# Kernel tuning notes

Measured on AMD Instinct MI355X. Metric: run time of the kernel, lower is better.

The kernel has to match this reference:

```python
import jax, jax.numpy as jnp
import numpy as np

N_NODES = 50000
N_EDGES = 400000
F_IN = 128
HID = 64
HEADS = 8
N_CLASSES = 16
NEG_SLOPE = 0.2  # PyG GATConv default negative_slope


def _glorot(key, shape):
    fan_in, fan_out = shape[0], shape[-1]
    lim = jnp.sqrt(6.0 / (fan_in + fan_out))
    return jax.random.uniform(key, shape, jnp.float32, -lim, lim)


def setup_inputs() -> dict:
    key = jax.random.key(0)
    ks = jax.random.split(key, 16)
    x = jax.random.normal(ks[0], (N_NODES, F_IN), jnp.float32)
    edge_index = jax.random.randint(ks[1], (2, N_EDGES), 0, N_NODES, jnp.int64)
    # layer 0: F_IN -> HEADS*HID (concat)
    W0 = _glorot(ks[2], (F_IN, HEADS * HID))
    a_s0 = _glorot(ks[3], (HEADS, HID))
    a_d0 = _glorot(ks[4], (HEADS, HID))
    b0 = jnp.zeros((HEADS * HID,), jnp.float32)
    # layer 1: HEADS*HID -> HEADS*HID (concat)
    W1 = _glorot(ks[5], (HEADS * HID, HEADS * HID))
    a_s1 = _glorot(ks[6], (HEADS, HID))
    a_d1 = _glorot(ks[7], (HEADS, HID))
    b1 = jnp.zeros((HEADS * HID,), jnp.float32)
    # final layer: HEADS*HID -> N_CLASSES, heads=1, concat=False (mean over heads)
    W2 = _glorot(ks[8], (HEADS * HID, 1 * N_CLASSES))
    a_s2 = _glorot(ks[9], (1, N_CLASSES))
    a_d2 = _glorot(ks[10], (1, N_CLASSES))
    b2 = jnp.zeros((N_CLASSES,), jnp.float32)
    return {"x": x, "edge_index": edge_index,
            "W0": W0, "a_s0": a_s0, "a_d0": a_d0, "b0": b0,
            "W1": W1, "a_s1": a_s1, "a_d1": a_d1, "b1": b1,
            "W2": W2, "a_s2": a_s2, "a_d2": a_d2, "b2": b2}


def gat_conv(x, src, dst, W, a_src, a_dst, b, num_nodes, concat):
    """One PyG-style GATConv (self-loops already in src/dst).
    x: [N, F_in]; W: [F_in, H*C]; a_src/a_dst: [H, C]; b: [H*C] or [C]."""
    H, C = a_src.shape
    h = (x @ W).reshape(num_nodes, H, C)                    # [N,H,C]
    al_s = jnp.einsum('nhc,hc->nh', h, a_src)               # [N,H]
    al_d = jnp.einsum('nhc,hc->nh', h, a_dst)               # [N,H]
    e = jax.nn.leaky_relu(al_s[src] + al_d[dst], NEG_SLOPE) # [E,H]
    # scatter-softmax over incoming edges of each destination node
    m = jax.ops.segment_max(e, dst, num_segments=num_nodes)  # [N,H]
    ex = jnp.exp(e - m[dst])
    denom = jax.ops.segment_sum(ex, dst, num_segments=num_nodes)
    alpha = ex / denom[dst]                                  # [E,H]
    out = jax.ops.segment_sum(alpha[:, :, None] * h[src], dst,
                              num_segments=num_nodes)        # [N,H,C]
    if concat:
        return out.reshape(num_nodes, H * C) + b
    return out.mean(axis=1) + b


def reference(x, edge_index, W0, a_s0, a_d0, b0, W1, a_s1, a_d1, b1,
              W2, a_s2, a_d2, b2):
    N = x.shape[0]
    # PyG GATConv adds self-loops by default
    loops = jnp.arange(N, dtype=edge_index.dtype)
    src = jnp.concatenate([edge_index[0], loops])
    dst = jnp.concatenate([edge_index[1], loops])
    h = gat_conv(x, src, dst, W0, a_s0, a_d0, b0, N, concat=True)
    h = jax.nn.elu(h)  # dropout is identity in eval mode
    h = gat_conv(h, src, dst, W1, a_s1, a_d1, b1, N, concat=True)
    h = jax.nn.elu(h)
    return gat_conv(h, src, dst, W2, a_s2, a_d2, b2, N, concat=False)
```

## Files before the change

kernel.cpp:

```cpp
#include <hip/hip_runtime.h>

#define N_NODES 50000
#define N_EDGES 400000
#define E_TOT   450000
#define NEG 0.2f
#define NB_SCAN ((N_NODES + 255) / 256)
#define MAXD 64

typedef unsigned short ushort_t;
typedef __attribute__((ext_vector_type(8))) _Float16 half8;
typedef __attribute__((ext_vector_type(4))) float  f32x4;
typedef __attribute__((ext_vector_type(8))) unsigned short ushort8;

__device__ __forceinline__ ushort_t f2h(float f){
    _Float16 h = (_Float16)f;
    union { _Float16 h; ushort_t u; } v; v.h = h; return v.u;
}
__device__ __forceinline__ float h_lo(unsigned u){
    union { unsigned u; _Float16 h[2]; } v; v.u = u; return (float)v.h[0];
}
__device__ __forceinline__ float h_hi(unsigned u){
    union { unsigned u; _Float16 h[2]; } v; v.u = u; return (float)v.h[1];
}
__device__ __forceinline__ void gload_lds16(const void* g, void* l){
    __builtin_amdgcn_global_load_lds((const __attribute__((address_space(1))) void*)g,
                                     (__attribute__((address_space(3))) void*)l, 16, 0, 0);
}
__device__ __forceinline__ int wave_incl_scan(int v, int lane){
    #pragma unroll
    for(int off = 1; off < 64; off <<= 1){
        int t = __shfl_up(v, off, 64);
        if(lane >= off) v += t;
    }
    return v;
}


__global__ void cvt_all(const float* __restrict__ W0,
                        const float* __restrict__ W1, const float* __restrict__ W2,
                        const int* __restrict__ ei,
                        ushort_t* __restrict__ W0t,
                        ushort_t* __restrict__ W1t, ushort_t* __restrict__ W2t,
                        int* __restrict__ deg){
    int i = blockIdx.x*256 + threadIdx.x;
    if(i < 512*128){ int n = i >> 7, k = i & 127; W0t[i] = f2h(W0[(size_t)k*512 + n]); }
    if(i < 512*512){ int n = i >> 9, k = i & 511; W1t[i] = f2h(W1[(size_t)k*512 + n]); }
    if(i < 16*512){ int n = i >> 9, k = i & 511; W2t[i] = f2h(W2[(size_t)k*16 + n]); }
    if(i < E_TOT){
        int dst = (i < N_EDGES) ? ei[N_EDGES + i] : (i - N_EDGES);
        atomicAdd(&deg[dst], 1);
    }
}


__global__ void deg_block_sum(const int* __restrict__ deg, int* __restrict__ bsum){
    int i = blockIdx.x*256 + threadIdx.x;
    int lane = threadIdx.x & 63, wave = threadIdx.x >> 6;
    int v = (i < N_NODES) ? deg[i] : 0;
    #pragma unroll
    for(int off = 1; off < 64; off <<= 1) v += __shfl_xor(v, off, 64);
    __shared__ int sw[4];
    if(lane == 0) sw[wave] = v;
    __syncthreads();
    if(threadIdx.x == 0) bsum[blockIdx.x] = sw[0] + sw[1] + sw[2] + sw[3];
}

__global__ void scan_apply(const int* __restrict__ bsum,
                           int* __restrict__ dw, int* __restrict__ rowptr){
    __shared__ int soff;
    __shared__ int sw[4];
    int i = blockIdx.x*256 + threadIdx.x;
    int lane = threadIdx.x & 63, wave = threadIdx.x >> 6;
    if(wave == 0){
        int s = 0;
        for(int j = lane; j < (int)blockIdx.x; j += 64) s += bsum[j];
        #pragma unroll
        for(int off = 1; off < 64; off <<= 1) s += __shfl_xor(s, off, 64);
        if(lane == 0) soff = s;
    }
    int v = (i < N_NODES) ? dw[i] : 0;
    int incl = wave_incl_scan(v, lane);
    if(lane == 63) sw[wave] = incl;
    __syncthreads();
    int add = soff;
    for(int w = 0; w < wave; w++) add += sw[w];
    int excl = incl - v + add;
    if(i < N_NODES){ rowptr[i] = excl; dw[i] = excl; }
    if(i == N_NODES-1) rowptr[N_NODES] = excl + v;
}

__global__ void scatter_edges(const int* __restrict__ ei, int* __restrict__ wofs,
                              int* __restrict__ csr){
    int e = blockIdx.x*256 + threadIdx.x;
    if(e >= E_TOT) return;
    int src, dst;
    if(e < N_EDGES){ src = ei[e]; dst = ei[N_EDGES + e]; }
    else { src = dst = e - N_EDGES; }
    int pos = atomicAdd(&wofs[dst], 1);
    csr[pos] = src;
}


__global__ __launch_bounds__(512, 2) void gemm0f(const float* __restrict__ x,
                                                 const ushort_t* __restrict__ W0t,
                                                 ushort_t* __restrict__ Cb,
                                                 const float* __restrict__ a_s,
                                                 const float* __restrict__ a_d,
                                                 float* __restrict__ als,
                                                 float* __restrict__ ald, int M){
    extern __shared__ ushort_t lds[];
    ushort_t* As = lds;
    ushort_t* Bs = lds + 128*128;
    int tid = threadIdx.x, wave = tid >> 6, lane = tid & 63;
    int row0 = blockIdx.x * 128;

    {
        int rsub = lane >> 4, c16 = lane & 15;
        #pragma unroll
        for(int s = 0; s < 16; s++){
            int rowq = wave*64 + s*4;
            int r = rowq + rsub;
            int sc = c16 ^ (r & 7);
            gload_lds16(W0t + (size_t)r*128 + sc*8, Bs + rowq*128);
        }
    }
    {
        int rsub = lane >> 4, c16 = lane & 15;
        #pragma unroll
        for(int t = 0; t < 4; t++){
            int rl = wave*16 + t*4 + rsub;
            int gr = row0 + rl; gr = gr < M ? gr : M-1;
            const float* ap = x + (size_t)gr*128 + c16*8;
            f32x4 lo = *(const f32x4*)ap;
            f32x4 hi = *(const f32x4*)(ap + 4);
            union { _Float16 h[8]; half8 v; } u;
            u.h[0] = (_Float16)lo[0]; u.h[1] = (_Float16)lo[1];
            u.h[2] = (_Float16)lo[2]; u.h[3] = (_Float16)lo[3];
            u.h[4] = (_Float16)hi[0]; u.h[5] = (_Float16)hi[1];
            u.h[6] = (_Float16)hi[2]; u.h[7] = (_Float16)hi[3];
            *(half8*)&As[(size_t)rl*128 + (c16 ^ (rl & 7))*8] = u.v;
        }
    }

    __syncthreads();

    f32x4 acc[8][4] = {};
    int fm = lane & 15, fq = lane >> 4;
    #pragma unroll
    for(int kt = 0; kt < 4; kt++){
        half8 a[8], b[4];
        #pragma unroll
        for(int mi = 0; mi < 8; mi++){
            int r = mi*16 + fm;
            a[mi] = *(const half8*)&As[(size_t)r*128 + ((kt*4 + fq) ^ (r & 7))*8];
        }
        #pragma unroll
        for(int nj = 0; nj < 4; nj++){
            int r = wave*64 + nj*16 + fm;
            b[nj] = *(const half8*)&Bs[(size_t)r*128 + ((kt*4 + fq) ^ (r & 7))*8];
        }
        #pragma unroll
        for(int mi = 0; mi < 8; mi++)
            #pragma unroll
            for(int nj = 0; nj < 4; nj++)
                acc[mi][nj] = __builtin_amdgcn_mfma_f32_16x16x32_f16(a[mi], b[nj], acc[mi][nj], 0, 0, 0);
    }

    int head = wave;
    float asv[4], adv[4];
    #pragma unroll
    for(int nj = 0; nj < 4; nj++){
        int c = head*64 + nj*16 + fm;
        asv[nj] = a_s[c]; adv[nj] = a_d[c];
    }
    #pragma unroll
    for(int mi = 0; mi < 8; mi++){
        #pragma unroll
        for(int p2 = 0; p2 < 4; p2++){
            int r = row0 + mi*16 + fq*4 + p2;
            float ps = 0.f, pd = 0.f;
            if(r < M){
                ushort_t* cp = &Cb[(size_t)r*512 + head*64 + fm];
                #pragma unroll
                for(int nj = 0; nj < 4; nj++){
                    float v = acc[mi][nj][p2];
                    cp[nj*16] = f2h(v);
                    ps += v*asv[nj]; pd += v*adv[nj];
                }
            }
            #pragma unroll
            for(int off = 1; off < 16; off <<= 1){
                ps += __shfl_xor(ps, off);
                pd += __shfl_xor(pd, off);
            }
            if(fm == 0 && r < M){ als[r*8 + head] = ps; ald[r*8 + head] = pd; }
        }
    }
}


template<int K>
__global__ __launch_bounds__(512, 2) void gemm_bt8(const ushort_t* __restrict__ A,
                                                   const ushort_t* __restrict__ Bt,
                                                   ushort_t* __restrict__ Cb,
                                                   const float* __restrict__ a_s,
                                                   const float* __restrict__ a_d,
                                                   float* __restrict__ als,
                                                   float* __restrict__ ald, int M){
    extern __shared__ ushort_t lds[];
    constexpr int NT = K / 64;
    int tid = threadIdx.x, wave = tid >> 6, lane = tid & 63;
    int wm = wave >> 2, wn = wave & 3;

    int s = blockIdx.x, nb = gridDim.x;
    int cc = s & 7, kk = s >> 3;
    int q = nb >> 3, rr = nb & 7;
    int t = (cc < rr ? cc*(q+1) : rr*(q+1) + (cc-rr)*q) + kk;
    int row0 = (t >> 1) * 256;
    int col0 = (t & 1) * 256;

    int lr = lane >> 3;
    int cs8 = ((lane & 7) ^ lr) << 3;
    int arows[4], brows[4];
    #pragma unroll
    for(int i = 0; i < 4; i++){
        int r = row0 + (wave << 5) + (i << 3) + lr;
        arows[i] = r < M ? r : M-1;
        brows[i] = col0 + (wave << 5) + (i << 3) + lr;
    }

    int l15 = lane & 15, fq = lane >> 4;
    int xr = (lane & 7) << 4;
    int xco0 = ((fq << 4)      ) ^ xr;
    int xco1 = (64 | (fq << 4)) ^ xr;

    f32x4 acc[8][4] = {};

    auto stage = [&](int nbuf, int kt, int i){
        ushort_t* la = lds + nbuf*16384 + (wave << 11) + (i << 9);
        ushort_t* lb = lds + 32768 + nbuf*16384 + (wave << 11) + (i << 9);
        gload_lds16(A  + (size_t)arows[i]*K + kt + cs8, la);
        gload_lds16(Bt + (size_t)brows[i]*K + kt + cs8, lb);
    };

    #pragma unroll
    for(int i = 0; i < 4; i++) stage(0, 0, i);
    #pragma unroll
    for(int i = 0; i < 4; i++) stage(1, 64, i);

    for(int it = 0; it < NT; ++it){
        int b = it & 1;
        if(it < NT-1) asm volatile("s_waitcnt vmcnt(8)" ::: "memory");
        else         asm volatile("s_waitcnt vmcnt(0)" ::: "memory");
        __builtin_amdgcn_s_barrier();
        const char* Ac = (const char*)(lds + b*16384);
        const char* Bc = (const char*)(lds + 32768 + b*16384);
        #pragma unroll
        for(int p = 0; p < 4; ++p){
            half8 aF[2][2], bF[4][2];
            #pragma unroll
            for(int m2 = 0; m2 < 2; m2++){
                int ro = (((wm << 7) + (((p << 1) | m2) << 4) + l15)) << 7;
                aF[m2][0] = *(const half8*)(Ac + ro + xco0);
                aF[m2][1] = *(const half8*)(Ac + ro + xco1);
            }
            #pragma unroll
            for(int nj = 0; nj < 4; nj++){
                int ro = (((wn << 6) + (nj << 4) + l15)) << 7;
                bF[nj][0] = *(const half8*)(Bc + ro + xco0);
                bF[nj][1] = *(const half8*)(Bc + ro + xco1);
            }
            if(p == 3) asm volatile("s_waitcnt lgkmcnt(0)" ::: "memory");
            __builtin_amdgcn_s_barrier();
            if(p == 3 && it < NT-2){
                #pragma unroll
                for(int i = 0; i < 4; i++) stage(b, (it + 2) << 6, i);
            }
            __builtin_amdgcn_s_setprio(1);
            #pragma unroll
            for(int m2 = 0; m2 < 2; m2++)
                #pragma unroll
                for(int nj = 0; nj < 4; nj++){
                    acc[(p<<1)|m2][nj] = __builtin_amdgcn_mfma_f32_16x16x32_f16(aF[m2][0], bF[nj][0], acc[(p<<1)|m2][nj], 0, 0, 0);
                    acc[(p<<1)|m2][nj] = __builtin_amdgcn_mfma_f32_16x16x32_f16(aF[m2][1], bF[nj][1], acc[(p<<1)|m2][nj], 0, 0, 0);
                }
            __builtin_amdgcn_s_setprio(0);
            __builtin_amdgcn_s_barrier();
        }
    }

    int head = (col0 >> 6) + wn;
    float asv[4], adv[4];
    #pragma unroll
    for(int nj = 0; nj < 4; nj++){
        int c = (head << 6) + (nj << 4) + l15;
        asv[nj] = a_s[c]; adv[nj] = a_d[c];
    }
    #pragma unroll
    for(int mi = 0; mi < 8; mi++){
        #pragma unroll
        for(int p2 = 0; p2 < 4; p2++){
            int r = row0 + (wm << 7) + (mi << 4) + (fq << 2) + p2;
            float ps = 0.f, pd = 0.f;
            if(r < M){
                ushort_t* cp = &Cb[(size_t)r*512 + (head << 6) + l15];
                #pragma unroll
                for(int nj = 0; nj < 4; nj++){
                    float v = acc[mi][nj][p2];
                    cp[nj << 4] = f2h(v);
                    ps += v*asv[nj]; pd += v*adv[nj];
                }
            }
            #pragma unroll
            for(int off = 1; off < 16; off <<= 1){
                ps += __shfl_xor(ps, off);
                pd += __shfl_xor(pd, off);
            }
            if(l15 == 0 && r < M){ als[r*8 + head] = ps; ald[r*8 + head] = pd; }
        }
    }
}


__global__ __launch_bounds__(256) void attn_agg(const ushort_t* __restrict__ h,
        const float* __restrict__ als, const float* __restrict__ ald,
        const int* __restrict__ rowptr, const int* __restrict__ csr,
        const float* __restrict__ bias, ushort_t* __restrict__ out){
    __shared__ float sex[4][MAXD][8];
    int wv = threadIdx.x >> 6, lane = threadIdx.x & 63;
    int n = blockIdx.x*4 + wv;
    int start = rowptr[n], end = rowptr[n+1];

    int hd = lane & 7, e8 = lane >> 3;
    float aldv = ald[n*8 + hd];
    float lmax = -1e30f;
    for(int idx = start + e8; idx < end; idx += 8){
        int e = idx - start;
        int src = csr[idx];
        float v = als[src*8 + hd] + aldv;
        v = v > 0.f ? v : NEG*v;
        if(e < MAXD) sex[wv][e][hd] = v;
        lmax = fmaxf(lmax, v);
    }
    for(int off = 8; off < 64; off <<= 1) lmax = fmaxf(lmax, __shfl_xor(lmax, off));
    float lsum = 0.f;
    for(int idx = start + e8; idx < end; idx += 8){
        int e = idx - start;
        float v;
        if(e < MAXD) v = sex[wv][e][hd];
        else { int src = csr[idx]; v = als[src*8 + hd] + aldv; v = v > 0.f ? v : NEG*v; }
        float ex = __expf(v - lmax);
        if(e < MAXD) sex[wv][e][hd] = ex;
        lsum += ex;
    }
    for(int off = 8; off < 64; off <<= 1) lsum += __shfl_xor(lsum, off);

    int head = e8;
    float m_all = __shfl(lmax, head);
    float inv   = 1.f / __shfl(lsum, head);
    float aldn  = __shfl(aldv, head);

    float acc[8] = {};

    int cnt = end - start;
    int nmain = cnt < MAXD ? cnt : MAXD;
    int mend = start + nmain;
    int last = mend - 1;
    for(int idx = start; idx < mend; idx += 8){
        int ss[8]; uint4 pp[8]; float ee[8];
        #pragma unroll
        for(int k = 0; k < 8; k++){
            int j = idx + k;
            ss[k] = csr[j <= last ? j : last];
        }
        #pragma unroll
        for(int k = 0; k < 8; k++)
            pp[k] = *(const uint4*)&h[(size_t)ss[k]*512 + lane*8];
        #pragma unroll
        for(int k = 0; k < 8; k++){
            int j = idx + k;
            ee[k] = (j < mend) ? sex[wv][j-start][head] : 0.f;
        }
        #pragma unroll
        for(int k = 0; k < 8; k++){
            acc[0] += ee[k]*h_lo(pp[k].x); acc[1] += ee[k]*h_hi(pp[k].x);
            acc[2] += ee[k]*h_lo(pp[k].y); acc[3] += ee[k]*h_hi(pp[k].y);
            acc[4] += ee[k]*h_lo(pp[k].z); acc[5] += ee[k]*h_hi(pp[k].z);
            acc[6] += ee[k]*h_lo(pp[k].w); acc[7] += ee[k]*h_hi(pp[k].w);
        }
    }
    if(mend < end){
        for(int idx = mend; idx < end; idx++){
            int src = csr[idx];
            float v = als[src*8 + head] + aldn;
            v = v > 0.f ? v : NEG*v;
            float e0 = __expf(v - m_all);
            uint4 p = *(const uint4*)&h[(size_t)src*512 + lane*8];
            acc[0] += e0*h_lo(p.x); acc[1] += e0*h_hi(p.x);
            acc[2] += e0*h_lo(p.y); acc[3] += e0*h_hi(p.y);
            acc[4] += e0*h_lo(p.z); acc[5] += e0*h_hi(p.z);
            acc[6] += e0*h_lo(p.w); acc[7] += e0*h_hi(p.w);
        }
    }

    ushort8 o;
    #pragma unroll
    for(int j = 0; j < 8; j++){
        float v = acc[j]*inv + bias[lane*8 + j];
        v = v > 0.f ? v : (__expf(v) - 1.f);
        o[j] = f2h(v);
    }
    *(ushort8*)&out[(size_t)n*512 + lane*8] = o;
}


__global__ __launch_bounds__(256) void gemm2_mfma(const ushort_t* __restrict__ A,
                                                  const ushort_t* __restrict__ W2t,
                                                  const float* __restrict__ a_s2,
                                                  const float* __restrict__ a_d2,
                                                  float* __restrict__ C,
                                                  float* __restrict__ als,
                                                  float* __restrict__ ald){
    int wave = threadIdx.x >> 6, lane = threadIdx.x & 63;
    long row0 = (long)(blockIdx.x*4 + wave)*16;
    int fr = lane & 15, fq = lane >> 4;
    long ar = row0 + fr;
    if(ar > N_NODES-1) ar = N_NODES-1;
    const ushort_t* ap = A + ar*512 + fq*8;
    const ushort_t* bp = W2t + (size_t)fr*512 + fq*8;
    f32x4 acc = {};
    #pragma unroll
    for(int kt = 0; kt < 512; kt += 32){
        half8 a = *(const half8*)(ap + kt);
        half8 b = *(const half8*)(bp + kt);
        acc = __builtin_amdgcn_mfma_f32_16x16x32_f16(a, b, acc, 0, 0, 0);
    }
    float as_ = a_s2[fr], ad_ = a_d2[fr];
    #pragma unroll
    for(int p = 0; p < 4; p++){
        long r = row0 + fq*4 + p;
        float v = acc[p];
        float ps = v*as_, pd = v*ad_;
        #pragma unroll
        for(int off = 1; off < 16; off <<= 1){
            ps += __shfl_xor(ps, off);
            pd += __shfl_xor(pd, off);
        }
        if(r < N_NODES){
            C[r*16 + fr] = v;
            if(fr == 0){ als[r] = ps; ald[r] = pd; }
        }
    }
}

__global__ __launch_bounds__(256) void attn_agg2(const float* __restrict__ h2,
        const float* __restrict__ als, const float* __restrict__ ald,
        const int* __restrict__ rowptr, const int* __restrict__ csr,
        const float* __restrict__ b2, float* __restrict__ out){
    __shared__ float sex2[16][MAXD+1];
    int wv = threadIdx.x >> 6, lane = threadIdx.x & 63;
    int q = lane >> 4, c = lane & 15;
    int slot = wv*4 + q;
    int n = blockIdx.x*16 + slot;
    int start = rowptr[n], end = rowptr[n+1];
    float aldv = ald[n];
    int cnt = end - start;
    int nmain = cnt < MAXD ? cnt : MAXD;
    int mend = start + nmain;

    float lmax = -1e30f;
    for(int idx = start + c; idx < end; idx += 16){
        int e = idx - start;
        float v = als[csr[idx]] + aldv; v = v > 0.f ? v : NEG*v;
        if(e < MAXD) sex2[slot][e] = v;
        lmax = fmaxf(lmax, v);
    }
    #pragma unroll
    for(int off = 1; off < 16; off <<= 1) lmax = fmaxf(lmax, __shfl_xor(lmax, off));
    float lsum = 0.f;
    for(int idx = start + c; idx < end; idx += 16){
        int e = idx - start;
        float v;
        if(e < MAXD) v = sex2[slot][e];
        else { v = als[csr[idx]] + aldv; v = v > 0.f ? v : NEG*v; }
        float ex = __expf(v - lmax);
        if(e < MAXD) sex2[slot][e] = ex;
        lsum += ex;
    }
    #pragma unroll
    for(int off = 1; off < 16; off <<= 1) lsum += __shfl_xor(lsum, off);
    float inv = 1.f / lsum;

    float acc = 0.f;
    for(int idx = start; idx < mend; idx++){
        int src = csr[idx];
        float ex = sex2[slot][idx - start];
        acc += ex * h2[(size_t)src*16 + c];
    }
    for(int idx = mend; idx < end; idx++){
        int src = csr[idx];
        float v = als[src] + aldv; v = v > 0.f ? v : NEG*v;
        acc += __expf(v - lmax) * h2[(size_t)src*16 + c];
    }
    out[(size_t)n*16 + c] = acc*inv + b2[c];
}


extern "C" void kernel_launch(void* const* d_in, const int* in_sizes, int n_in,
                              void* d_out, int out_size, void* d_ws, size_t ws_size,
                              hipStream_t stream) {
    const float* x    = (const float*)d_in[0];
    const int*   ei   = (const int*)  d_in[1];
    const float* W0   = (const float*)d_in[2];
    const float* a_s0 = (const float*)d_in[3];
    const float* a_d0 = (const float*)d_in[4];
    const float* b0   = (const float*)d_in[5];
    const float* W1   = (const float*)d_in[6];
    const float* a_s1 = (const float*)d_in[7];
    const float* a_d1 = (const float*)d_in[8];
    const float* b1   = (const float*)d_in[9];
    const float* W2   = (const float*)d_in[10];
    const float* a_s2 = (const float*)d_in[11];
    const float* a_d2 = (const float*)d_in[12];
    const float* b2   = (const float*)d_in[13];
    float* out = (float*)d_out;

    char* w = (char*)d_ws;
    auto alloc = [&](size_t bytes){ void* p = (void*)w; w += (bytes + 255) & ~(size_t)255; return p; };
    int*      rowptr = (int*)     alloc((N_NODES+1)*sizeof(int));
    int*      wofs   = (int*)     alloc((N_NODES+1)*sizeof(int));
    int*      bsum   = (int*)     alloc(NB_SCAN*sizeof(int));
    int*      csr    = (int*)     alloc(E_TOT*sizeof(int));
    float*    als    = (float*)   alloc((size_t)N_NODES*8*sizeof(float));
    float*    ald    = (float*)   alloc((size_t)N_NODES*8*sizeof(float));
    float*    als2   = (float*)   alloc((size_t)N_NODES*sizeof(float));
    float*    ald2   = (float*)   alloc((size_t)N_NODES*sizeof(float));
    ushort_t* hb     = (ushort_t*)alloc((size_t)N_NODES*512*sizeof(ushort_t));
    ushort_t* hbf    = (ushort_t*)alloc((size_t)N_NODES*512*sizeof(ushort_t));
    ushort_t* W0t    = (ushort_t*)alloc((size_t)512*128*sizeof(ushort_t));
    ushort_t* W1t    = (ushort_t*)alloc((size_t)512*512*sizeof(ushort_t));
    ushort_t* W2t    = (ushort_t*)alloc((size_t)16*512*sizeof(ushort_t));
    float*    h2     = (float*)   alloc((size_t)N_NODES*16*sizeof(float));

    const int NBLK = 2 * ((N_NODES + 255) / 256);
    const int NG0  = (N_NODES + 127) / 128;

    (void)hipFuncSetAttribute((const void*)gemm_bt8<512>,
                              hipFuncAttributeMaxDynamicSharedMemorySize, 131072);
    (void)hipFuncSetAttribute((const void*)gemm0f,
                              hipFuncAttributeMaxDynamicSharedMemorySize, 163840);

    hipMemsetAsync(wofs, 0, (N_NODES+1)*sizeof(int), stream);
    cvt_all<<<(E_TOT+255)/256, 256, 0, stream>>>(W0, W1, W2, ei, W0t, W1t, W2t, wofs);

    deg_block_sum<<<NB_SCAN, 256, 0, stream>>>(wofs, bsum);
    scan_apply<<<NB_SCAN, 256, 0, stream>>>(bsum, wofs, rowptr);
    scatter_edges<<<(E_TOT+255)/256, 256, 0, stream>>>(ei, wofs, csr);

    gemm0f<<<NG0, 512, 163840, stream>>>(x, W0t, hb, a_s0, a_d0, als, ald, N_NODES);
    attn_agg<<<N_NODES/4, 256, 0, stream>>>(hb, als, ald, rowptr, csr, b0, hbf);

    gemm_bt8<512><<<NBLK, 512, 131072, stream>>>(hbf, W1t, hb, a_s1, a_d1, als, ald, N_NODES);
    attn_agg<<<N_NODES/4, 256, 0, stream>>>(hb, als, ald, rowptr, csr, b1, hbf);

    gemm2_mfma<<<(N_NODES+63)/64, 256, 0, stream>>>(hbf, W2t, a_s2, a_d2, h2, als2, ald2);
    attn_agg2<<<N_NODES/16, 256, 0, stream>>>(h2, als2, ald2, rowptr, csr, b2, out);
}
```

Before: 419.5 us.

## Fuse CSR edge scatter into layer-0 GEMM and process two row tiles per block

Removes the separate scatter_edges launch and folds the edge-to-CSR atomic scatter into the first GEMM kernel, with each block handling a slice of edges while its W0/x tiles load. Each GEMM block now covers 256 rows in two 128-row passes, so W0 is staged into LDS once per block and the next A tile is staged while the previous epilogue runs. The grid drops to 196 blocks at one block per CU. That cuts parallelism and latency hiding and serialises the two tiles inside each block, in exchange for one fewer launch and less W0 reloading.

```diff
diff --git a/kernel.cpp b/kernel.cpp
--- a/kernel.cpp
+++ b/kernel.cpp
@@ -6,6 +6,8 @@
 #define NEG 0.2f
 #define NB_SCAN ((N_NODES + 255) / 256)
 #define MAXD 64
+#define NG0 196
+#define EPB ((E_TOT + NG0 - 1) / NG0)
 
 typedef unsigned short ushort_t;
 typedef __attribute__((ext_vector_type(8))) _Float16 half8;
@@ -89,48 +91,31 @@
     if(i == N_NODES-1) rowptr[N_NODES] = excl + v;
 }
 
-__global__ void scatter_edges(const int* __restrict__ ei, int* __restrict__ wofs,
-                              int* __restrict__ csr){
-    int e = blockIdx.x*256 + threadIdx.x;
-    if(e >= E_TOT) return;
-    int src, dst;
-    if(e < N_EDGES){ src = ei[e]; dst = ei[N_EDGES + e]; }
-    else { src = dst = e - N_EDGES; }
-    int pos = atomicAdd(&wofs[dst], 1);
-    csr[pos] = src;
-}
-
-
-__global__ __launch_bounds__(512, 2) void gemm0f(const float* __restrict__ x,
-                                                 const ushort_t* __restrict__ W0t,
-                                                 ushort_t* __restrict__ Cb,
-                                                 const float* __restrict__ a_s,
-                                                 const float* __restrict__ a_d,
-                                                 float* __restrict__ als,
-                                                 float* __restrict__ ald, int M){
+
+__global__ __launch_bounds__(512, 1) void gemm0fs(const int* __restrict__ ei,
+                                                  int* __restrict__ wofs,
+                                                  int* __restrict__ csr,
+                                                  const float* __restrict__ x,
+                                                  const ushort_t* __restrict__ W0t,
+                                                  ushort_t* __restrict__ Cb,
+                                                  const float* __restrict__ a_s,
+                                                  const float* __restrict__ a_d,
+                                                  float* __restrict__ als,
+                                                  float* __restrict__ ald, int M){
     extern __shared__ ushort_t lds[];
-    ushort_t* As = lds;
-    ushort_t* Bs = lds + 128*128;
+    ushort_t* Bs = lds;
+    ushort_t* As = lds + 512*128;
     int tid = threadIdx.x, wave = tid >> 6, lane = tid & 63;
-    int row0 = blockIdx.x * 128;
-
-    {
-        int rsub = lane >> 4, c16 = lane & 15;
-        #pragma unroll
-        for(int s = 0; s < 16; s++){
-            int rowq = wave*64 + s*4;
-            int r = rowq + rsub;
-            int sc = c16 ^ (r & 7);
-            gload_lds16(W0t + (size_t)r*128 + sc*8, Bs + rowq*128);
-        }
-    }
-    {
-        int rsub = lane >> 4, c16 = lane & 15;
+    int rsub = lane >> 4, c16 = lane & 15;
+    int fm = lane & 15, fq = lane >> 4;
+    long row0 = (long)blockIdx.x * 256;
+
+    auto stageA = [&](long base){
         #pragma unroll
         for(int t = 0; t < 4; t++){
             int rl = wave*16 + t*4 + rsub;
-            int gr = row0 + rl; gr = gr < M ? gr : M-1;
-            const float* ap = x + (size_t)gr*128 + c16*8;
+            long gr = base + rl; gr = gr < M ? gr : M-1;
+            const float* ap = x + gr*128 + c16*8;
             f32x4 lo = *(const f32x4*)ap;
             f32x4 hi = *(const f32x4*)(ap + 4);
             union { _Float16 h[8]; half8 v; } u;
@@ -140,62 +125,93 @@
             u.h[6] = (_Float16)hi[2]; u.h[7] = (_Float16)hi[3];
             *(half8*)&As[(size_t)rl*128 + (c16 ^ (rl & 7))*8] = u.v;
         }
+    };
+    auto compute = [&](f32x4 (&acc)[8][4]){
+        #pragma unroll
+        for(int kt = 0; kt < 4; kt++){
+            half8 a[8], b[4];
+            #pragma unroll
+            for(int mi = 0; mi < 8; mi++){
+                int r = mi*16 + fm;
+                a[mi] = *(const half8*)&As[(size_t)r*128 + ((kt*4 + fq) ^ (r & 7))*8];
+            }
+            #pragma unroll
+            for(int nj = 0; nj < 4; nj++){
+                int r = wave*64 + nj*16 + fm;
+                b[nj] = *(const half8*)&Bs[(size_t)r*128 + ((kt*4 + fq) ^ (r & 7))*8];
+            }
+            #pragma unroll
+            for(int mi = 0; mi < 8; mi++)
+                #pragma unroll
+                for(int nj = 0; nj < 4; nj++)
+                    acc[mi][nj] = __builtin_amdgcn_mfma_f32_16x16x32_f16(a[mi], b[nj], acc[mi][nj], 0, 0, 0);
+        }
+    };
+    auto epilogue = [&](f32x4 (&acc)[8][4], long base){
+        int head = wave;
+        float asv[4], adv[4];
+        #pragma unroll
+        for(int nj = 0; nj < 4; nj++){
+            int c = head*64 + nj*16 + fm;
+            asv[nj] = a_s[c]; adv[nj] = a_d[c];
+        }
+        #pragma unroll
+        for(int mi = 0; mi < 8; mi++){
+            #pragma unroll
+            for(int p2 = 0; p2 < 4; p2++){
+                long r = base + mi*16 + fq*4 + p2;
+                float ps = 0.f, pd = 0.f;
+                if(r < M){
+                    ushort_t* cp = &Cb[(size_t)r*512 + head*64 + fm];
+                    #pragma unroll
+                    for(int nj = 0; nj < 4; nj++){
+                        float v = acc[mi][nj][p2];
+                        cp[nj*16] = f2h(v);
+                        ps += v*asv[nj]; pd += v*adv[nj];
+                    }
+                }
+                #pragma unroll
+                for(int off = 1; off < 16; off <<= 1){
+                    ps += __shfl_xor(ps, off);
+                    pd += __shfl_xor(pd, off);
+                }
+                if(fm == 0 && r < M){ als[r*8 + head] = ps; ald[r*8 + head] = pd; }
+            }
+        }
+    };
+
+    #pragma unroll
+    for(int s = 0; s < 16; s++){
+        int rowq = wave*64 + s*4;
+        int r = rowq + rsub;
+        int sc = c16 ^ (r & 7);
+        gload_lds16(W0t + (size_t)r*128 + sc*8, Bs + rowq*128);
+    }
+    stageA(row0);
+
+    {
+        int e1 = blockIdx.x*EPB + EPB; if(e1 > E_TOT) e1 = E_TOT;
+        for(int e = blockIdx.x*EPB + tid; e < e1; e += 512){
+            int src, dst;
+            if(e < N_EDGES){ src = ei[e]; dst = ei[N_EDGES + e]; }
+            else { src = dst = e - N_EDGES; }
+            int pos = atomicAdd(&wofs[dst], 1);
+            csr[pos] = src;
+        }
     }
 
     __syncthreads();
 
     f32x4 acc[8][4] = {};
-    int fm = lane & 15, fq = lane >> 4;
-    #pragma unroll
-    for(int kt = 0; kt < 4; kt++){
-        half8 a[8], b[4];
-        #pragma unroll
-        for(int mi = 0; mi < 8; mi++){
-            int r = mi*16 + fm;
-            a[mi] = *(const half8*)&As[(size_t)r*128 + ((kt*4 + fq) ^ (r & 7))*8];
-        }
-        #pragma unroll
-        for(int nj = 0; nj < 4; nj++){
-            int r = wave*64 + nj*16 + fm;
-            b[nj] = *(const half8*)&Bs[(size_t)r*128 + ((kt*4 + fq) ^ (r & 7))*8];
-        }
-        #pragma unroll
-        for(int mi = 0; mi < 8; mi++)
-            #pragma unroll
-            for(int nj = 0; nj < 4; nj++)
-                acc[mi][nj] = __builtin_amdgcn_mfma_f32_16x16x32_f16(a[mi], b[nj], acc[mi][nj], 0, 0, 0);
-    }
-
-    int head = wave;
-    float asv[4], adv[4];
-    #pragma unroll
-    for(int nj = 0; nj < 4; nj++){
-        int c = head*64 + nj*16 + fm;
-        asv[nj] = a_s[c]; adv[nj] = a_d[c];
-    }
-    #pragma unroll
-    for(int mi = 0; mi < 8; mi++){
-        #pragma unroll
-        for(int p2 = 0; p2 < 4; p2++){
-            int r = row0 + mi*16 + fq*4 + p2;
-            float ps = 0.f, pd = 0.f;
-            if(r < M){
-                ushort_t* cp = &Cb[(size_t)r*512 + head*64 + fm];
-                #pragma unroll
-                for(int nj = 0; nj < 4; nj++){
-                    float v = acc[mi][nj][p2];
-                    cp[nj*16] = f2h(v);
-                    ps += v*asv[nj]; pd += v*adv[nj];
-                }
-            }
-            #pragma unroll
-            for(int off = 1; off < 16; off <<= 1){
-                ps += __shfl_xor(ps, off);
-                pd += __shfl_xor(pd, off);
-            }
-            if(fm == 0 && r < M){ als[r*8 + head] = ps; ald[r*8 + head] = pd; }
-        }
-    }
+    compute(acc);
+    __syncthreads();
+    stageA(row0 + 128);
+    epilogue(acc, row0);
+    __syncthreads();
+
+    f32x4 acc2[8][4] = {};
+    compute(acc2);
+    epilogue(acc2, row0 + 128);
 }
 
 
@@ -543,11 +559,10 @@
     float*    h2     = (float*)   alloc((size_t)N_NODES*16*sizeof(float));
 
     const int NBLK = 2 * ((N_NODES + 255) / 256);
-    const int NG0  = (N_NODES + 127) / 128;
 
     (void)hipFuncSetAttribute((const void*)gemm_bt8<512>,
                               hipFuncAttributeMaxDynamicSharedMemorySize, 131072);
-    (void)hipFuncSetAttribute((const void*)gemm0f,
+    (void)hipFuncSetAttribute((const void*)gemm0fs,
                               hipFuncAttributeMaxDynamicSharedMemorySize, 163840);
 
     hipMemsetAsync(wofs, 0, (N_NODES+1)*sizeof(int), stream);
@@ -555,9 +570,8 @@
 
     deg_block_sum<<<NB_SCAN, 256, 0, stream>>>(wofs, bsum);
     scan_apply<<<NB_SCAN, 256, 0, stream>>>(bsum, wofs, rowptr);
-    scatter_edges<<<(E_TOT+255)/256, 256, 0, stream>>>(ei, wofs, csr);
-
-    gemm0f<<<NG0, 512, 163840, stream>>>(x, W0t, hb, a_s0, a_d0, als, ald, N_NODES);
+
+    gemm0fs<<<NG0, 512, 163840, stream>>>(ei, wofs, csr, x, W0t, hb, a_s0, a_d0, als, ald, N_NODES);
     attn_agg<<<N_NODES/4, 256, 0, stream>>>(hb, als, ald, rowptr, csr, b0, hbf);
 
     gemm_bt8<512><<<NBLK, 512, 131072, stream>>>(hbf, W1t, hb, a_s1, a_d1, als, ald, N_NODES);
```

After: 416.0 us. No clear change (-0.8%).
